# Optimization experiments

Measured on AMD Instinct MI355X. Metric: run time of the kernel, lower is better.

## Reference

```python
import jax, jax.numpy as jnp
import numpy as np

B, T, I, H = 256, 256, 2048, 128

def setup_inputs() -> dict:
    key = jax.random.key(0)
    ks = jax.random.split(key, 7)
    s = 1.0 / np.sqrt(H)  # torch RNN/Linear init scale
    return {
        "x": jax.random.normal(ks[0], (B, T, I), dtype=jnp.float32),
        "W_ih": jax.random.uniform(ks[1], (H, I), jnp.float32, -s, s),
        "W_hh": jax.random.uniform(ks[2], (H, H), jnp.float32, -s, s),
        "b_ih": jax.random.uniform(ks[3], (H,), jnp.float32, -s, s),
        "b_hh": jax.random.uniform(ks[4], (H,), jnp.float32, -s, s),
        "W_fc": jax.random.uniform(ks[5], (1, H), jnp.float32, -s, s),
        "b_fc": jax.random.uniform(ks[6], (1,), jnp.float32, -s, s),
    }

def reference(x, W_ih, W_hh, b_ih, b_hh, W_fc, b_fc):
    # Precompute input projection for all timesteps as one big GEMM: [B,T,H]
    xp = jnp.einsum('bti,hi->bth', x, W_ih) + (b_ih + b_hh)
    h0 = jnp.zeros((x.shape[0], W_hh.shape[0]), dtype=x.dtype)

    def step(h, xt):  # xt: [B,H]
        h = jnp.tanh(xt + h @ W_hh.T)
        return h, None

    hT, _ = jax.lax.scan(step, h0, jnp.swapaxes(xp, 0, 1))  # final hidden [B,H]
    out = hT @ W_fc.T + b_fc  # [B,1]
    return out.squeeze(1)     # [B]
```

## Files before the change

### kernel.cpp

```cpp
#include <hip/hip_runtime.h>
#include <hip/hip_bf16.h>
#include <math.h>

#define B_ 256
#define T_ 256
#define I_ 2048
#define H_ 128

#define BM 128
#define BK 32
#define NKT (I_ / BK)

typedef __attribute__((ext_vector_type(8))) short bf16x8;
typedef __attribute__((ext_vector_type(4))) float f32x4;

static __device__ inline short f2bf(float f) {
    __hip_bfloat16 h = __float2bfloat16(f);
    return *reinterpret_cast<short*>(&h);
}

static __device__ inline bf16x8 pack8(float4 a, float4 b) {
    bf16x8 r;
    r[0] = f2bf(a.x); r[1] = f2bf(a.y); r[2] = f2bf(a.z); r[3] = f2bf(a.w);
    r[4] = f2bf(b.x); r[5] = f2bf(b.y); r[6] = f2bf(b.z); r[7] = f2bf(b.w);
    return r;
}

__global__ __launch_bounds__(256, 2) void proj_mfma(
    const float* __restrict__ x, const float* __restrict__ Wih,
    const float* __restrict__ bih, const float* __restrict__ bhh,
    float* __restrict__ xp)
{
    __shared__ __align__(16) float As[2][BM * BK];
    __shared__ __align__(16) float Bs[2][H_ * BK];

    const int tid  = threadIdx.x;
    const int lane = tid & 63;
    const int wid  = tid >> 6;
    const int wr   = wid >> 1;
    const int wc   = wid & 1;
    const long row0 = (long)blockIdx.x * BM;

    const int srow  = lane >> 3;
    const int sunit = (lane & 7) ^ srow;

    f32x4 acc[4][4];
    #pragma unroll
    for (int m = 0; m < 4; ++m)
        #pragma unroll
        for (int n = 0; n < 4; ++n)
            acc[m][n] = (f32x4){0.f, 0.f, 0.f, 0.f};

    const int fr = lane & 15;
    const int fq = lane >> 4;

    const int rb0 = wid * 32;

    #pragma unroll
    for (int i = 0; i < 4; ++i) {
        const int rbase = rb0 + i * 8;
        const float* ga = x   + (row0 + rbase + srow) * I_ + sunit * 4;
        const float* gb = Wih + (long)(rbase + srow) * I_ + sunit * 4;
        __builtin_amdgcn_global_load_lds(
            (const __attribute__((address_space(1))) void*)ga,
            (__attribute__((address_space(3))) void*)&As[0][rbase * BK], 16, 0, 0);
        __builtin_amdgcn_global_load_lds(
            (const __attribute__((address_space(1))) void*)gb,
            (__attribute__((address_space(3))) void*)&Bs[0][rbase * BK], 16, 0, 0);
    }
    __syncthreads();

    int p = 0;
    for (int t = 0; t < NKT; ++t) {
        if (t + 1 < NKT) {
            const int kk = (t + 1) * BK;
            #pragma unroll
            for (int i = 0; i < 4; ++i) {
                const int rbase = rb0 + i * 8;
                const float* ga = x   + (row0 + rbase + srow) * I_ + kk + sunit * 4;
                const float* gb = Wih + (long)(rbase + srow) * I_ + kk + sunit * 4;
                __builtin_amdgcn_global_load_lds(
                    (const __attribute__((address_space(1))) void*)ga,
                    (__attribute__((address_space(3))) void*)&As[p ^ 1][rbase * BK], 16, 0, 0);
                __builtin_amdgcn_global_load_lds(
                    (const __attribute__((address_space(1))) void*)gb,
                    (__attribute__((address_space(3))) void*)&Bs[p ^ 1][rbase * BK], 16, 0, 0);
            }
        }
        bf16x8 af[4], bfr[4];
        #pragma unroll
        for (int f = 0; f < 4; ++f) {
            const int ra_ = wr * 64 + f * 16 + fr;
            const float4 a0 = *reinterpret_cast<const float4*>(
                &As[p][ra_ * BK + (((fq * 2)     ^ (ra_ & 7)) * 4)]);
            const float4 a1 = *reinterpret_cast<const float4*>(
                &As[p][ra_ * BK + (((fq * 2 + 1) ^ (ra_ & 7)) * 4)]);
            af[f] = pack8(a0, a1);
            const int rb_ = wc * 64 + f * 16 + fr;
            const float4 b0 = *reinterpret_cast<const float4*>(
                &Bs[p][rb_ * BK + (((fq * 2)     ^ (rb_ & 7)) * 4)]);
            const float4 b1 = *reinterpret_cast<const float4*>(
                &Bs[p][rb_ * BK + (((fq * 2 + 1) ^ (rb_ & 7)) * 4)]);
            bfr[f] = pack8(b0, b1);
        }
        #pragma unroll
        for (int m = 0; m < 4; ++m)
            #pragma unroll
            for (int n = 0; n < 4; ++n)
                acc[m][n] = __builtin_amdgcn_mfma_f32_16x16x32_bf16(
                    af[m], bfr[n], acc[m][n], 0, 0, 0);
        __syncthreads();
        p ^= 1;
    }

    #pragma unroll
    for (int n = 0; n < 4; ++n) {
        const int col = wc * 64 + n * 16 + fr;
        const float bn = bih[col] + bhh[col];
        #pragma unroll
        for (int m = 0; m < 4; ++m) {
            const long rbase = row0 + wr * 64 + m * 16 + fq * 4;
            #pragma unroll
            for (int j = 0; j < 4; ++j)
                xp[(rbase + j) * H_ + col] = acc[m][n][j] + bn;
        }
    }
}

__global__ __launch_bounds__(256) void scan_kernel(
    const float* __restrict__ xp, const float* __restrict__ Whh,
    const float* __restrict__ Wfc, const float* __restrict__ bfc,
    float* __restrict__ out)
{
    __shared__ __align__(16) float hbuf[2][H_];

    const int tid  = threadIdx.x;
    const int lane = tid & 63;
    const int w    = tid >> 6;
    const int j    = w * 32 + (lane & 31);
    const int g    = lane >> 5;
    const int b    = blockIdx.x;

    float Wreg[64];
    {
        const float4* wp = reinterpret_cast<const float4*>(&Whh[(long)j * H_ + g * 64]);
        #pragma unroll
        for (int q = 0; q < 16; ++q) {
            const float4 wv = wp[q];
            Wreg[4*q]   = wv.x; Wreg[4*q+1] = wv.y;
            Wreg[4*q+2] = wv.z; Wreg[4*q+3] = wv.w;
        }
    }
    if (tid < H_) hbuf[0][tid] = 0.f;

    const float* xprow = xp + (long)b * T_ * H_ + j;
    float xa = xprow[0 * H_];
    float xb = xprow[1 * H_];
    float xc = xprow[2 * H_];
    float xd = xprow[3 * H_];
    __syncthreads();

    auto body = [&](int t, float xpv) {
        const float4* h4 = reinterpret_cast<const float4*>(&hbuf[t & 1][g * 64]);
        float a0 = 0.f, a1 = 0.f, a2 = 0.f, a3 = 0.f;
        #pragma unroll
        for (int q = 0; q < 16; ++q) {
            const float4 hh = h4[q];
            a0 += hh.x * Wreg[4*q];
            a1 += hh.y * Wreg[4*q+1];
            a2 += hh.z * Wreg[4*q+2];
            a3 += hh.w * Wreg[4*q+3];
        }
        float part = (a0 + a1) + (a2 + a3);
        part += __shfl_xor(part, 32);
        const float pre = part + xpv;
        const float e = __expf(2.f * pre);
        hbuf[(t + 1) & 1][j] = 1.f - 2.f / (e + 1.f);
        __syncthreads();
    };

    for (int t = 0; t < T_; t += 4) {
        float xu;
        xu = xa; if (t + 4 < T_) xa = xprow[(long)(t + 4) * H_];
        body(t + 0, xu);
        xu = xb; if (t + 5 < T_) xb = xprow[(long)(t + 5) * H_];
        body(t + 1, xu);
        xu = xc; if (t + 6 < T_) xc = xprow[(long)(t + 6) * H_];
        body(t + 2, xu);
        xu = xd; if (t + 7 < T_) xd = xprow[(long)(t + 7) * H_];
        body(t + 3, xu);
    }

    if (w == 0) {
        float v = hbuf[0][lane] * Wfc[lane] + hbuf[0][lane + 64] * Wfc[lane + 64];
        #pragma unroll
        for (int off = 32; off > 0; off >>= 1) v += __shfl_down(v, off);
        if (lane == 0) out[b] = v + bfc[0];
    }
}

extern "C" void kernel_launch(void* const* d_in, const int* in_sizes, int n_in,
                              void* d_out, int out_size, void* d_ws, size_t ws_size,
                              hipStream_t stream)
{
    const float* x   = (const float*)d_in[0];
    const float* Wih = (const float*)d_in[1];
    const float* Whh = (const float*)d_in[2];
    const float* bih = (const float*)d_in[3];
    const float* bhh = (const float*)d_in[4];
    const float* Wfc = (const float*)d_in[5];
    const float* bfc = (const float*)d_in[6];
    float* out = (float*)d_out;
    float* xp  = (float*)d_ws;

    proj_mfma<<<dim3((B_ * T_) / BM), dim3(256), 0, stream>>>(x, Wih, bih, bhh, xp);
    scan_kernel<<<dim3(B_), dim3(256), 0, stream>>>(xp, Whh, Wfc, bfc, out);
}
```

Before: 271.1 us.

## Run scan as single wavefront with fp16 packed dot2 recurrence

The recurrent scan moves from a 256-thread block to one 64-lane wavefront per batch element. Each lane computes two hidden units using fp16 weights held in registers and fdot2 instructions, and the hidden state is stored as packed halves in LDS. This replaces the per-step block-wide __syncthreads and cross-lane shuffle with a cheap wave barrier and halves the LDS traffic. The cost is fp16 rounding of W_hh and h over 256 steps, which adds accuracy risk, and more serial work per lane.

```diff
diff --git a/kernel.cpp b/kernel.cpp
--- a/kernel.cpp
+++ b/kernel.cpp
@@ -13,6 +13,7 @@
 
 typedef __attribute__((ext_vector_type(8))) short bf16x8;
 typedef __attribute__((ext_vector_type(4))) float f32x4;
+typedef _Float16 half2v __attribute__((ext_vector_type(2)));
 
 static __device__ inline short f2bf(float f) {
     __hip_bfloat16 h = __float2bfloat16(f);
@@ -53,7 +54,6 @@
 
     const int fr = lane & 15;
     const int fq = lane >> 4;
-
     const int rb0 = wid * 32;
 
     #pragma unroll
@@ -127,75 +127,93 @@
     }
 }
 
-__global__ __launch_bounds__(256) void scan_kernel(
+__global__ __launch_bounds__(64, 1) void scan_kernel(
     const float* __restrict__ xp, const float* __restrict__ Whh,
     const float* __restrict__ Wfc, const float* __restrict__ bfc,
     float* __restrict__ out)
 {
-    __shared__ __align__(16) float hbuf[2][H_];
-
-    const int tid  = threadIdx.x;
-    const int lane = tid & 63;
-    const int w    = tid >> 6;
-    const int j    = w * 32 + (lane & 31);
-    const int g    = lane >> 5;
-    const int b    = blockIdx.x;
-
-    float Wreg[64];
+    __shared__ __align__(16) unsigned hpk[2][H_ / 2];
+
+    const int l = threadIdx.x;
+    const int b = blockIdx.x;
+    const int j0 = 2 * l;
+
+    half2v W0[64], W1[64];
     {
-        const float4* wp = reinterpret_cast<const float4*>(&Whh[(long)j * H_ + g * 64]);
+        const float4* w0 = reinterpret_cast<const float4*>(&Whh[(long)j0 * H_]);
+        const float4* w1 = reinterpret_cast<const float4*>(&Whh[(long)(j0 + 1) * H_]);
+        #pragma unroll
+        for (int q = 0; q < 32; ++q) {
+            const float4 a = w0[q];
+            const float4 c = w1[q];
+            half2v p0, p1, p2, p3;
+            p0[0] = (_Float16)a.x; p0[1] = (_Float16)a.y;
+            p1[0] = (_Float16)a.z; p1[1] = (_Float16)a.w;
+            p2[0] = (_Float16)c.x; p2[1] = (_Float16)c.y;
+            p3[0] = (_Float16)c.z; p3[1] = (_Float16)c.w;
+            W0[2 * q] = p0; W0[2 * q + 1] = p1;
+            W1[2 * q] = p2; W1[2 * q + 1] = p3;
+        }
+    }
+    hpk[0][l] = 0u;
+    __builtin_amdgcn_wave_barrier();
+
+    const float2* xprow2 = reinterpret_cast<const float2*>(xp + (long)b * T_ * H_) + l;
+    float2 xa = xprow2[0 * 64];
+    float2 xb = xprow2[1 * 64];
+    float2 xc = xprow2[2 * 64];
+    float2 xd = xprow2[3 * 64];
+
+    auto body = [&](int t, float2 xpv) {
+        const uint4* hp = reinterpret_cast<const uint4*>(&hpk[t & 1][0]);
+        float a0 = 0.f, a1 = 0.f, c0 = 0.f, c1 = 0.f;
         #pragma unroll
         for (int q = 0; q < 16; ++q) {
-            const float4 wv = wp[q];
-            Wreg[4*q]   = wv.x; Wreg[4*q+1] = wv.y;
-            Wreg[4*q+2] = wv.z; Wreg[4*q+3] = wv.w;
-        }
-    }
-    if (tid < H_) hbuf[0][tid] = 0.f;
-
-    const float* xprow = xp + (long)b * T_ * H_ + j;
-    float xa = xprow[0 * H_];
-    float xb = xprow[1 * H_];
-    float xc = xprow[2 * H_];
-    float xd = xprow[3 * H_];
-    __syncthreads();
-
-    auto body = [&](int t, float xpv) {
-        const float4* h4 = reinterpret_cast<const float4*>(&hbuf[t & 1][g * 64]);
-        float a0 = 0.f, a1 = 0.f, a2 = 0.f, a3 = 0.f;
-        #pragma unroll
-        for (int q = 0; q < 16; ++q) {
-            const float4 hh = h4[q];
-            a0 += hh.x * Wreg[4*q];
-            a1 += hh.y * Wreg[4*q+1];
-            a2 += hh.z * Wreg[4*q+2];
-            a3 += hh.w * Wreg[4*q+3];
-        }
-        float part = (a0 + a1) + (a2 + a3);
-        part += __shfl_xor(part, 32);
-        const float pre = part + xpv;
-        const float e = __expf(2.f * pre);
-        hbuf[(t + 1) & 1][j] = 1.f - 2.f / (e + 1.f);
-        __syncthreads();
+            const uint4 u = hp[q];
+            const half2v h0 = __builtin_bit_cast(half2v, u.x);
+            const half2v h1 = __builtin_bit_cast(half2v, u.y);
+            const half2v h2 = __builtin_bit_cast(half2v, u.z);
+            const half2v h3 = __builtin_bit_cast(half2v, u.w);
+            a0 = __builtin_amdgcn_fdot2(h0, W0[4*q+0], a0, false);
+            a1 = __builtin_amdgcn_fdot2(h1, W0[4*q+1], a1, false);
+            a0 = __builtin_amdgcn_fdot2(h2, W0[4*q+2], a0, false);
+            a1 = __builtin_amdgcn_fdot2(h3, W0[4*q+3], a1, false);
+            c0 = __builtin_amdgcn_fdot2(h0, W1[4*q+0], c0, false);
+            c1 = __builtin_amdgcn_fdot2(h1, W1[4*q+1], c1, false);
+            c0 = __builtin_amdgcn_fdot2(h2, W1[4*q+2], c0, false);
+            c1 = __builtin_amdgcn_fdot2(h3, W1[4*q+3], c1, false);
+        }
+        const float pre0 = (a0 + a1) + xpv.x;
+        const float pre1 = (c0 + c1) + xpv.y;
+        const float e0 = __expf(2.f * pre0);
+        const float e1 = __expf(2.f * pre1);
+        half2v hh;
+        hh[0] = (_Float16)(1.f - 2.f / (e0 + 1.f));
+        hh[1] = (_Float16)(1.f - 2.f / (e1 + 1.f));
+        hpk[(t + 1) & 1][l] = __builtin_bit_cast(unsigned, hh);
+        __builtin_amdgcn_wave_barrier();
     };
 
     for (int t = 0; t < T_; t += 4) {
-        float xu;
-        xu = xa; if (t + 4 < T_) xa = xprow[(long)(t + 4) * H_];
+        float2 xu;
+        xu = xa; if (t + 4 < T_) xa = xprow2[(long)(t + 4) * 64];
         body(t + 0, xu);
-        xu = xb; if (t + 5 < T_) xb = xprow[(long)(t + 5) * H_];
+        xu = xb; if (t + 5 < T_) xb = xprow2[(long)(t + 5) * 64];
         body(t + 1, xu);
-        xu = xc; if (t + 6 < T_) xc = xprow[(long)(t + 6) * H_];
+        xu = xc; if (t + 6 < T_) xc = xprow2[(long)(t + 6) * 64];
         body(t + 2, xu);
-        xu = xd; if (t + 7 < T_) xd = xprow[(long)(t + 7) * H_];
+        xu = xd; if (t + 7 < T_) xd = xprow2[(long)(t + 7) * 64];
         body(t + 3, xu);
     }
 
-    if (w == 0) {
-        float v = hbuf[0][lane] * Wfc[lane] + hbuf[0][lane + 64] * Wfc[lane + 64];
+    {
+        const unsigned u = hpk[0][l];
+        const half2v hh = __builtin_bit_cast(half2v, u);
+        const float2 wf = reinterpret_cast<const float2*>(Wfc)[l];
+        float v = (float)hh[0] * wf.x + (float)hh[1] * wf.y;
         #pragma unroll
         for (int off = 32; off > 0; off >>= 1) v += __shfl_down(v, off);
-        if (lane == 0) out[b] = v + bfc[0];
+        if (l == 0) out[b] = v + bfc[0];
     }
 }
 
@@ -214,5 +232,5 @@
     float* xp  = (float*)d_ws;
 
     proj_mfma<<<dim3((B_ * T_) / BM), dim3(256), 0, stream>>>(x, Wih, bih, bhh, xp);
-    scan_kernel<<<dim3(B_), dim3(256), 0, stream>>>(xp, Whh, Wfc, bfc, out);
-}
+    scan_kernel<<<dim3(B_), dim3(64), 0, stream>>>(xp, Whh, Wfc, bfc, out);
+}
```

Result: faster. 251.8 us (-7.1%).
